# Kernel optimization log

Hardware: AMD Instinct MI355X
Metric: run time of the kernel (lower is better)

Reference implementation:

```python
import jax, jax.numpy as jnp
import numpy as np


def _pairwise_dist(A, B):
    # Euclidean cdist via ||a||^2 + ||b||^2 - 2 a.b, avoiding a [B,N,M,D] intermediate.
    a2 = jnp.sum(A * A, axis=-1)  # [b, n]
    b2 = jnp.sum(B * B, axis=-1)  # [b, m]
    ab = jnp.einsum('bnd,bmd->bnm', A, B)  # [b, n, m]
    sq = a2[:, :, None] + b2[:, None, :] - 2.0 * ab
    return jnp.sqrt(jnp.maximum(sq, 0.0))


def setup_inputs() -> dict:
    key = jax.random.key(0)
    kA, kB = jax.random.split(key)
    A = jax.random.normal(kA, (4, 8192, 3), dtype=jnp.float32)
    B = jax.random.normal(kB, (4, 8192, 3), dtype=jnp.float32)
    return {"A": A, "B": B}


def reference(A, B):
    d = _pairwise_dist(A, B)              # [b, n, m]
    min_a2b = jnp.min(d, axis=2)          # [b, n]
    min_b2a = jnp.min(d, axis=1)          # [b, m]
    chamfer = jnp.mean(min_a2b, axis=1) + jnp.mean(min_b2a, axis=1)  # [b]
    return jnp.mean(chamfer) / 12.8
```

## Files before the change

kernel.cpp:

```cpp
#include <hip/hip_runtime.h>


typedef __bf16 bf16x8 __attribute__((ext_vector_type(8)));
typedef float f32x16 __attribute__((ext_vector_type(16)));
typedef unsigned short u16;

constexpr int NB = 4;
constexpr int NPTS = 8192;
constexpr int NROWS = 2 * NB * NPTS;
constexpr int FRAGS = 4;
constexpr int ROWS_PER_BLK = FRAGS * 32;
constexpr int ROWBLKS = NPTS / ROWS_PER_BLK;
constexpr int SSPLIT = 4;
constexpr int SPTS = NPTS / SSPLIT;
constexpr int TILES_PER_WAVE = SPTS / 32 / 4;
constexpr int DEPTH = 4;

constexpr size_t REST_OFF = 2u << 20;
constexpr size_t WSMIN_OFF = 4u << 20;

__device__ __forceinline__ float bsplit(float x, u16& hbits, float& hf) {
    unsigned u = __float_as_uint(x);
    unsigned r = (u + 0x7FFFu + ((u >> 16) & 1u)) & 0xFFFF0000u;
    hbits = (u16)(r >> 16);
    hf = __uint_as_float(r);
    return x - hf;
}

__global__ __launch_bounds__(256)
void chamfer_prep_kernel(const float* __restrict__ A, const float* __restrict__ B,
                         u16* __restrict__ streamT, u16* __restrict__ resT,
                         unsigned int* __restrict__ ws_min) {
    int idx = blockIdx.x * 256 + threadIdx.x;
    int pt = idx & (NPTS - 1);
    int batch = (idx >> 13) & (NB - 1);
    int set = idx >> 15;
    const float* src = (set ? B : A) + ((size_t)batch * NPTS + pt) * 3;
    float x = src[0], y = src[1], z = src[2];
    float s2 = fmaf(x, x, fmaf(y, y, z * z));
    float hf, h2;
    u16 s2h, s2l, s2ll, xh, xl, yh, yl, zh, zl, mxh, mxl, myh, myl, mzh, mzl;
    float r1 = bsplit(s2, s2h, hf);
    float r2 = bsplit(r1, s2l, h2);
    bsplit(r2, s2ll, h2);
    float t;
    t = bsplit(x, xh, hf);          bsplit(t, xl, h2);
    t = bsplit(y, yh, hf);          bsplit(t, yl, h2);
    t = bsplit(z, zh, hf);          bsplit(t, zl, h2);
    t = bsplit(-2.0f * x, mxh, hf); bsplit(t, mxl, h2);
    t = bsplit(-2.0f * y, myh, hf); bsplit(t, myl, h2);
    t = bsplit(-2.0f * z, mzh, hf); bsplit(t, mzl, h2);
    const unsigned ONE = 0x3F80u;
    #define PK(a, b) ((unsigned)(a) | ((unsigned)(b) << 16))
    uint4 rw0 = make_uint4(PK(s2h, s2l), PK(s2ll, ONE), PK(ONE, ONE), PK(mxh, myh));
    uint4 rw1 = make_uint4(PK(mzh, mxh), PK(myh, mzh), PK(mxl, myl), PK(mzl, 0));
    uint4 cw0 = make_uint4(PK(ONE, ONE), PK(ONE, s2h), PK(s2l, s2ll), PK(xh, yh));
    uint4 cw1 = make_uint4(PK(zh, xl), PK(yl, zl), PK(xh, yh), PK(zh, 0));
    #undef PK
    uint4* sp = (uint4*)(streamT + (size_t)idx * 16);
    uint4* rp = (uint4*)(resT + (size_t)idx * 16);
    sp[0] = rw0; sp[1] = rw1;
    rp[0] = cw0; rp[1] = cw1;
    ws_min[idx] = 0xFFFFFFFFu;
}

__device__ __forceinline__ float tree16(const f32x16& d) {
    float m0 = fminf(fminf(d[0],  d[1]),  d[2]);
    float m1 = fminf(fminf(d[3],  d[4]),  d[5]);
    float m2 = fminf(fminf(d[6],  d[7]),  d[8]);
    float m3 = fminf(fminf(d[9],  d[10]), d[11]);
    float m4 = fminf(fminf(d[12], d[13]), d[14]);
    float n0 = fminf(fminf(m0, m1), m2);
    float n1 = fminf(fminf(m3, m4), d[15]);
    return fminf(n0, n1);
}

__global__ __launch_bounds__(256, 4)
void chamfer_minmfma_kernel(const u16* __restrict__ streamT,
                            const u16* __restrict__ resT,
                            unsigned int* __restrict__ ws_min) {
    int bid = blockIdx.x;
    int split  = bid & (SSPLIT - 1);  bid >>= 2;
    int rowblk = bid & (ROWBLKS - 1); bid >>= 6;
    int batch  = bid & (NB - 1);      bid >>= 2;
    int dir    = bid;

    int lane = threadIdx.x & 63;
    int wave = threadIdx.x >> 6;
    int l31 = lane & 31, lh = lane >> 5;

    const u16* rbase = resT + (((size_t)(dir * NB + batch) * NPTS) + rowblk * ROWS_PER_BLK) * 16;
    bf16x8 res[FRAGS];
    #pragma unroll
    for (int f = 0; f < FRAGS; ++f)
        res[f] = *(const bf16x8*)(rbase + (f * 32 + l31) * 16 + lh * 8);

    const uint4* wp = (const uint4*)streamT
                    + (size_t)((dir ^ 1) * NB + batch) * NPTS * 2
                    + (size_t)split * SPTS * 2
                    + (size_t)wave * TILES_PER_WAVE * 64
                    + (l31 * 2 + lh);

    f32x16 zf;
    #pragma unroll
    for (int j = 0; j < 16; ++j) zf[j] = 0.0f;
    float accf[FRAGS];
    #pragma unroll
    for (int f = 0; f < FRAGS; ++f) accf[f] = 3.0e38f;

    uint4 pipe[DEPTH];
    #pragma unroll
    for (int i = 0; i < DEPTH; ++i) pipe[i] = wp[i * 64];

    for (int t = 0; t < TILES_PER_WAVE; t += DEPTH) {
        #pragma unroll
        for (int u = 0; u < DEPTH; ++u) {
            uint4 cur = pipe[u];
            pipe[u] = wp[(t + u + DEPTH) * 64];
            bf16x8 aop = __builtin_bit_cast(bf16x8, cur);
            #pragma unroll
            for (int f = 0; f < FRAGS; ++f) {
                f32x16 d = __builtin_amdgcn_mfma_f32_32x32x16_bf16(aop, res[f], zf, 0, 0, 0);
                accf[f] = fminf(accf[f], tree16(d));
            }
        }
    }

    unsigned int* wout = ws_min + (size_t)(dir * NB + batch) * NPTS + rowblk * ROWS_PER_BLK;
    #pragma unroll
    for (int f = 0; f < FRAGS; ++f) {
        float v = fminf(accf[f], __shfl_xor(accf[f], 32, 64));
        v = fmaxf(v, 0.0f);
        if (lh == 0) atomicMin(&wout[f * 32 + l31], __float_as_uint(v));
    }
}

__global__ __launch_bounds__(256)
void chamfer_reduce_kernel(const unsigned int* __restrict__ ws_min,
                           float* __restrict__ out) {
    constexpr float SCALE = 1.0f / (NB * NPTS * 12.8f);
    int idx = (blockIdx.x * 256 + threadIdx.x) * 4;
    uint4 v = *(const uint4*)(ws_min + idx);
    float s = sqrtf(__uint_as_float(v.x)) + sqrtf(__uint_as_float(v.y))
            + sqrtf(__uint_as_float(v.z)) + sqrtf(__uint_as_float(v.w));
    #pragma unroll
    for (int off = 32; off >= 1; off >>= 1) s += __shfl_down(s, off, 64);
    __shared__ float redl[4];
    if ((threadIdx.x & 63) == 0) redl[threadIdx.x >> 6] = s;
    __syncthreads();
    if (threadIdx.x == 0)
        atomicAdd(out, (redl[0] + redl[1] + redl[2] + redl[3]) * SCALE);
}

extern "C" void kernel_launch(void* const* d_in, const int* in_sizes, int n_in,
                              void* d_out, int out_size, void* d_ws, size_t ws_size,
                              hipStream_t stream) {
    const float* A = (const float*)d_in[0];
    const float* B = (const float*)d_in[1];
    float* out = (float*)d_out;
    u16* streamT = (u16*)d_ws;
    u16* resT = (u16*)((char*)d_ws + REST_OFF);
    unsigned int* wsm = (unsigned int*)((char*)d_ws + WSMIN_OFF);

    hipMemsetAsync(d_out, 0, sizeof(float), stream);
    chamfer_prep_kernel<<<NROWS / 256, 256, 0, stream>>>(A, B, streamT, resT, wsm);
    chamfer_minmfma_kernel<<<2 * NB * ROWBLKS * SSPLIT, 256, 0, stream>>>(streamT, resT, wsm);
    chamfer_reduce_kernel<<<NROWS / 4 / 256, 256, 0, stream>>>(wsm, out);
}
```

Baseline: 36.82 us.

## Double per-block row fragments and interleave MFMA with min-reduction trees

Each block now keeps eight 32-row resident fragments instead of four, so every streamed tile is reused across twice as many MFMAs and the total stream traffic is halved. The inner loop is unrolled by hand into two alternating MFMA result registers, so each min-tree runs while the next MFMA executes. The block index decode is also reordered so that direction and batch vary fastest. In exchange, the grid has half as many blocks, each doing more work, and the kernel uses more registers, which may reduce occupancy and load balance.

```diff
diff --git a/kernel.cpp b/kernel.cpp
--- a/kernel.cpp
+++ b/kernel.cpp
@@ -8,7 +8,7 @@
 constexpr int NB = 4;
 constexpr int NPTS = 8192;
 constexpr int NROWS = 2 * NB * NPTS;
-constexpr int FRAGS = 4;
+constexpr int FRAGS = 8;
 constexpr int ROWS_PER_BLK = FRAGS * 32;
 constexpr int ROWBLKS = NPTS / ROWS_PER_BLK;
 constexpr int SSPLIT = 4;
@@ -64,7 +64,7 @@
     ws_min[idx] = 0xFFFFFFFFu;
 }
 
-__device__ __forceinline__ float tree16(const f32x16& d) {
+__device__ __forceinline__ float tree16acc(const f32x16& d, float acc) {
     float m0 = fminf(fminf(d[0],  d[1]),  d[2]);
     float m1 = fminf(fminf(d[3],  d[4]),  d[5]);
     float m2 = fminf(fminf(d[6],  d[7]),  d[8]);
@@ -72,28 +72,33 @@
     float m4 = fminf(fminf(d[12], d[13]), d[14]);
     float n0 = fminf(fminf(m0, m1), m2);
     float n1 = fminf(fminf(m3, m4), d[15]);
-    return fminf(n0, n1);
+    return fminf(fminf(n0, n1), acc);
 }
 
 __global__ __launch_bounds__(256, 4)
 void chamfer_minmfma_kernel(const u16* __restrict__ streamT,
                             const u16* __restrict__ resT,
                             unsigned int* __restrict__ ws_min) {
-    int bid = blockIdx.x;
-    int split  = bid & (SSPLIT - 1);  bid >>= 2;
-    int rowblk = bid & (ROWBLKS - 1); bid >>= 6;
-    int batch  = bid & (NB - 1);      bid >>= 2;
-    int dir    = bid;
+    int db     = blockIdx.x & 7;
+    int rest   = blockIdx.x >> 3;
+    int split  = rest & (SSPLIT - 1);
+    int rowblk = rest >> 2;
+    int batch  = db & (NB - 1);
+    int dir    = db >> 2;
 
     int lane = threadIdx.x & 63;
     int wave = threadIdx.x >> 6;
     int l31 = lane & 31, lh = lane >> 5;
 
     const u16* rbase = resT + (((size_t)(dir * NB + batch) * NPTS) + rowblk * ROWS_PER_BLK) * 16;
-    bf16x8 res[FRAGS];
-    #pragma unroll
-    for (int f = 0; f < FRAGS; ++f)
-        res[f] = *(const bf16x8*)(rbase + (f * 32 + l31) * 16 + lh * 8);
+    bf16x8 res0 = *(const bf16x8*)(rbase + (0 * 32 + l31) * 16 + lh * 8);
+    bf16x8 res1 = *(const bf16x8*)(rbase + (1 * 32 + l31) * 16 + lh * 8);
+    bf16x8 res2 = *(const bf16x8*)(rbase + (2 * 32 + l31) * 16 + lh * 8);
+    bf16x8 res3 = *(const bf16x8*)(rbase + (3 * 32 + l31) * 16 + lh * 8);
+    bf16x8 res4 = *(const bf16x8*)(rbase + (4 * 32 + l31) * 16 + lh * 8);
+    bf16x8 res5 = *(const bf16x8*)(rbase + (5 * 32 + l31) * 16 + lh * 8);
+    bf16x8 res6 = *(const bf16x8*)(rbase + (6 * 32 + l31) * 16 + lh * 8);
+    bf16x8 res7 = *(const bf16x8*)(rbase + (7 * 32 + l31) * 16 + lh * 8);
 
     const uint4* wp = (const uint4*)streamT
                     + (size_t)((dir ^ 1) * NB + batch) * NPTS * 2
@@ -104,9 +109,8 @@
     f32x16 zf;
     #pragma unroll
     for (int j = 0; j < 16; ++j) zf[j] = 0.0f;
-    float accf[FRAGS];
-    #pragma unroll
-    for (int f = 0; f < FRAGS; ++f) accf[f] = 3.0e38f;
+    float acc0 = 3.0e38f, acc1 = 3.0e38f, acc2 = 3.0e38f, acc3 = 3.0e38f;
+    float acc4 = 3.0e38f, acc5 = 3.0e38f, acc6 = 3.0e38f, acc7 = 3.0e38f;
 
     uint4 pipe[DEPTH];
     #pragma unroll
@@ -118,18 +122,30 @@
             uint4 cur = pipe[u];
             pipe[u] = wp[(t + u + DEPTH) * 64];
             bf16x8 aop = __builtin_bit_cast(bf16x8, cur);
-            #pragma unroll
-            for (int f = 0; f < FRAGS; ++f) {
-                f32x16 d = __builtin_amdgcn_mfma_f32_32x32x16_bf16(aop, res[f], zf, 0, 0, 0);
-                accf[f] = fminf(accf[f], tree16(d));
-            }
+            f32x16 dA = __builtin_amdgcn_mfma_f32_32x32x16_bf16(aop, res0, zf, 0, 0, 0);
+            f32x16 dB = __builtin_amdgcn_mfma_f32_32x32x16_bf16(aop, res1, zf, 0, 0, 0);
+            acc0 = tree16acc(dA, acc0);
+            dA = __builtin_amdgcn_mfma_f32_32x32x16_bf16(aop, res2, zf, 0, 0, 0);
+            acc1 = tree16acc(dB, acc1);
+            dB = __builtin_amdgcn_mfma_f32_32x32x16_bf16(aop, res3, zf, 0, 0, 0);
+            acc2 = tree16acc(dA, acc2);
+            dA = __builtin_amdgcn_mfma_f32_32x32x16_bf16(aop, res4, zf, 0, 0, 0);
+            acc3 = tree16acc(dB, acc3);
+            dB = __builtin_amdgcn_mfma_f32_32x32x16_bf16(aop, res5, zf, 0, 0, 0);
+            acc4 = tree16acc(dA, acc4);
+            dA = __builtin_amdgcn_mfma_f32_32x32x16_bf16(aop, res6, zf, 0, 0, 0);
+            acc5 = tree16acc(dB, acc5);
+            dB = __builtin_amdgcn_mfma_f32_32x32x16_bf16(aop, res7, zf, 0, 0, 0);
+            acc6 = tree16acc(dA, acc6);
+            acc7 = tree16acc(dB, acc7);
         }
     }
 
     unsigned int* wout = ws_min + (size_t)(dir * NB + batch) * NPTS + rowblk * ROWS_PER_BLK;
+    float accs[FRAGS] = {acc0, acc1, acc2, acc3, acc4, acc5, acc6, acc7};
     #pragma unroll
     for (int f = 0; f < FRAGS; ++f) {
-        float v = fminf(accf[f], __shfl_xor(accf[f], 32, 64));
+        float v = fminf(accs[f], __shfl_xor(accs[f], 32, 64));
         v = fmaxf(v, 0.0f);
         if (lh == 0) atomicMin(&wout[f * 32 + l31], __float_as_uint(v));
     }
```

New measurement: 33.73 us. 1.09x faster.
